# Kernel tuning notes

Hardware: AMD Instinct MI355X
Metric: run time of the kernel (lower is better)

The kernel has to match this reference:

```python
import jax, jax.numpy as jnp
import numpy as np
import math

POOL = 7
NUM_CLASSES = 91
NMS_THRESH = 0.5
SCORE_THRESH = 0.05
TOPK = 100
DW_MAX = math.log(1000.0 / 16)


def _roi_pool(feat, rois, scale):
    # feat [C,H,W]; rois [N,4] xyxy in image coords. Matches torchvision.ops.roi_pool quantization.
    C, H, W = feat.shape
    N = rois.shape[0]
    r = jnp.round(rois * scale)
    x1, y1, x2, y2 = r[:, 0], r[:, 1], r[:, 2], r[:, 3]
    roi_w = jnp.maximum(x2 - x1 + 1.0, 1.0)
    roi_h = jnp.maximum(y2 - y1 + 1.0, 1.0)
    pb = jnp.arange(POOL, dtype=feat.dtype)
    hstart = jnp.clip(jnp.floor(pb[None, :] * roi_h[:, None] / POOL) + y1[:, None], 0, H)
    hend = jnp.clip(jnp.ceil((pb[None, :] + 1) * roi_h[:, None] / POOL) + y1[:, None], 0, H)
    wstart = jnp.clip(jnp.floor(pb[None, :] * roi_w[:, None] / POOL) + x1[:, None], 0, W)
    wend = jnp.clip(jnp.ceil((pb[None, :] + 1) * roi_w[:, None] / POOL) + x1[:, None], 0, W)
    hs = jnp.arange(H, dtype=feat.dtype)
    ws = jnp.arange(W, dtype=feat.dtype)
    mask_h = (hs >= hstart[..., None]) & (hs < hend[..., None])  # [N,P,H]
    mask_w = (ws >= wstart[..., None]) & (ws < wend[..., None])  # [N,P,W]
    NEG = jnp.asarray(-1e30, feat.dtype)

    def pool_one(mh, mw):
        # separable masked max: first over W, then over H
        t = jnp.where(mw[None, None, :, :], feat[:, :, None, :], NEG).max(-1)  # [C,H,P]
        o = jnp.where(mh[None, :, :, None], t[:, None, :, :], NEG).max(2)      # [C,P,P]
        empty = (~mh.any(-1))[:, None] | (~mw.any(-1))[None, :]                 # empty bins -> 0
        return jnp.where(empty[None], jnp.zeros((), feat.dtype), o)

    CH = 8  # chunk proposals to bound peak memory of the [C,H,P,W] intermediate
    mh = mask_h.reshape(N // CH, CH, POOL, H)
    mw = mask_w.reshape(N // CH, CH, POOL, W)
    pooled = jax.lax.map(lambda ms: jax.vmap(pool_one)(ms[0], ms[1]), (mh, mw))
    return pooled.reshape(N, C, POOL, POOL)


def _pairwise_iou(b1, b2):
    a1 = (b1[:, 2] - b1[:, 0]) * (b1[:, 3] - b1[:, 1])
    a2 = (b2[:, 2] - b2[:, 0]) * (b2[:, 3] - b2[:, 1])
    xl = jnp.maximum(b1[:, None, 0], b2[:, 0])
    yt = jnp.maximum(b1[:, None, 1], b2[:, 1])
    xr = jnp.minimum(b1[:, None, 2], b2[:, 2])
    yb = jnp.minimum(b1[:, None, 3], b2[:, 3])
    inter = jnp.maximum(xr - xl, 0.0) * jnp.maximum(yb - yt, 0.0)
    return inter / (a1[:, None] + a2 - inter + 1e-9)


def setup_inputs() -> dict:
    key = jax.random.key(0)
    ks = jax.random.split(key, 10)
    feat = jax.random.normal(ks[0], (1, 256, 50, 50), jnp.float32)
    N = 2000
    cx = jax.random.uniform(ks[1], (N,)) * 800.0
    cy = jax.random.uniform(ks[2], (N,)) * 800.0
    bw = jax.random.uniform(ks[3], (N,)) * 280.0 + 20.0
    bh = jax.random.uniform(ks[4], (N,)) * 280.0 + 20.0
    x1 = jnp.clip(cx - bw / 2, 0.0, 798.0)
    y1 = jnp.clip(cy - bh / 2, 0.0, 798.0)
    x2 = jnp.clip(cx + bw / 2, x1 + 1.0, 800.0)
    y2 = jnp.clip(cy + bh / 2, y1 + 1.0, 800.0)
    proposals = jnp.stack([x1, y1, x2, y2], axis=1).astype(jnp.float32)
    D = 256 * POOL * POOL
    fc1_w = jax.random.normal(ks[5], (1024, D), jnp.float32) * 0.01
    fc2_w = jax.random.normal(ks[6], (1024, 1024), jnp.float32) * 0.01
    cls_w = jax.random.normal(ks[7], (NUM_CLASSES, 1024), jnp.float32) * 0.01
    reg_w = jax.random.normal(ks[8], (NUM_CLASSES * 4, 1024), jnp.float32) * 0.001
    return dict(feat=feat, proposals=proposals,
                fc1_w=fc1_w, fc1_b=jnp.zeros((1024,), jnp.float32),
                fc2_w=fc2_w, fc2_b=jnp.zeros((1024,), jnp.float32),
                cls_w=cls_w, cls_b=jnp.zeros((NUM_CLASSES,), jnp.float32),
                reg_w=reg_w, reg_b=jnp.zeros((NUM_CLASSES * 4,), jnp.float32),
                img_h=800, img_w=800)


def reference(feat, proposals, fc1_w, fc1_b, fc2_w, fc2_b, cls_w, cls_b, reg_w, reg_b, img_h, img_w):
    fmap = feat[0]
    fh, fw = fmap.shape[-2:]
    scale = min(fh / img_h, fw / img_w)
    N = proposals.shape[0]
    pooled = _roi_pool(fmap, proposals, scale).reshape(N, -1)
    x = jax.nn.relu(pooled @ fc1_w.T + fc1_b)
    x = jax.nn.relu(x @ fc2_w.T + fc2_b)
    cls_scores = x @ cls_w.T + cls_b
    reg = (x @ reg_w.T + reg_b).reshape(N, NUM_CLASSES, 4)
    probs = jax.nn.softmax(cls_scores, axis=-1)
    fg = probs[:, 1:]
    pred_scores = fg.max(-1)
    pred_labels = fg.argmax(-1) + 1
    sel = reg[jnp.arange(N), pred_labels]
    pw = proposals[:, 2] - proposals[:, 0]
    ph = proposals[:, 3] - proposals[:, 1]
    pcx = proposals[:, 0] + 0.5 * pw
    pcy = proposals[:, 1] + 0.5 * ph
    dx, dy = sel[:, 0], sel[:, 1]
    dw = jnp.minimum(sel[:, 2], DW_MAX)
    dh = jnp.minimum(sel[:, 3], DW_MAX)
    cx = dx * pw + pcx
    cy = dy * ph + pcy
    bw = jnp.exp(dw) * pw
    bh = jnp.exp(dh) * ph
    boxes = jnp.stack([
        jnp.clip(cx - 0.5 * bw, 0.0, img_w),
        jnp.clip(cy - 0.5 * bh, 0.0, img_h),
        jnp.clip(cx + 0.5 * bw, 0.0, img_w),
        jnp.clip(cy + 0.5 * bh, 0.0, img_h)], axis=1)
    widths = boxes[:, 2] - boxes[:, 0]
    heights = boxes[:, 3] - boxes[:, 1]
    valid = (pred_scores >= SCORE_THRESH) & (widths >= 1.0) & (heights >= 1.0)
    # batched greedy NMS via per-class coordinate offset (torchvision batched_nms)
    sb = jax.lax.stop_gradient(boxes)
    offs = pred_labels.astype(boxes.dtype) * (sb.max() + 1.0)
    ob = sb + offs[:, None]
    order = jnp.argsort(jnp.where(valid, -pred_scores, jnp.inf))
    ob_s = ob[order]
    v_s = valid[order]
    iou = _pairwise_iou(ob_s, ob_s)
    idxs = jnp.arange(N)

    def body(i, supp):
        keep_i = v_s[i] & (~supp[i])
        return supp | (keep_i & (iou[i] > NMS_THRESH) & (idxs > i))

    supp = jax.lax.fori_loop(0, N, body, jnp.zeros((N,), bool))
    keep = v_s & (~supp)
    masked = jnp.where(keep, pred_scores[order], -jnp.inf)
    topv, topi = jax.lax.top_k(masked, TOPK)
    sel_idx = order[topi]
    ok = topv > -jnp.inf
    out_boxes = jnp.where(ok[:, None], boxes[sel_idx], 0.0)
    out_scores = jnp.where(ok, pred_scores[sel_idx], 0.0)
    out_labels = jnp.where(ok, pred_labels[sel_idx], 0)
    return out_boxes, out_labels, out_scores
```

## Files before the change

kernel.cpp:

```cpp
#include <hip/hip_runtime.h>
#include <cstdint>

#define POOLK 7
#define NCLS 91
#define FH 50
#define FW 50
#define FCH 256
#define DIM (FCH * POOLK * POOLK)
#define HID 1024
#define TOPK_OUT 100
#define DW_MAXF 4.135166556742356f

typedef __attribute__((ext_vector_type(8))) short short8;
typedef __attribute__((ext_vector_type(4))) float f32x4;

__device__ __forceinline__ unsigned short f2bf(float x)
{
    unsigned u = __float_as_uint(x);
    return (unsigned short)((u + 0x7FFFu + ((u >> 16) & 1u)) >> 16);
}

__global__ __launch_bounds__(256) void ftrans_kernel(
    const float* __restrict__ feat, float* __restrict__ featT)
{
    __shared__ float tile[64][65];
    int c0 = blockIdx.x * 64;
    int p0 = blockIdx.y * 64;
    int lane = threadIdx.x & 63, r4 = threadIdx.x >> 6;
    #pragma unroll
    for (int r = r4; r < 64; r += 4) {
        int p = p0 + lane;
        if (p < FH * FW) tile[r][lane] = feat[(size_t)(c0 + r) * (FH * FW) + p];
    }
    __syncthreads();
    #pragma unroll
    for (int r = r4; r < 64; r += 4) {
        int p = p0 + r;
        if (p < FH * FW) featT[(size_t)p * FCH + c0 + lane] = tile[lane][r];
    }
}

__global__ __launch_bounds__(512) void roi_pool_kernel(
    const float* __restrict__ featT, const float* __restrict__ props,
    unsigned short* __restrict__ pooled, int n0, int rows,
    const int* __restrict__ img_h, const int* __restrict__ img_w)
{
    int rl = blockIdx.x;
    if (rl >= rows) return;
    int n = n0 + rl;
    int lane = threadIdx.x & 63;
    int wv = threadIdx.x >> 6;

    float scale = (float)fmin((double)FH / (double)img_h[0],
                              (double)FW / (double)img_w[0]);
    float x1 = rintf(props[n * 4 + 0] * scale);
    float y1 = rintf(props[n * 4 + 1] * scale);
    float x2 = rintf(props[n * 4 + 2] * scale);
    float y2 = rintf(props[n * 4 + 3] * scale);
    float roiw = fmaxf(x2 - x1 + 1.f, 1.f);
    float roih = fmaxf(y2 - y1 + 1.f, 1.f);

    const float4* ft4 = (const float4*)featT;
    unsigned short* orow = pooled + (size_t)rl * DIM;

    for (int cell = wv; cell < 49; cell += 8) {
        int py = cell / 7, px = cell - py * 7;
        int h0 = (int)fminf(fmaxf(floorf((float)py * roih / 7.f) + y1, 0.f), (float)FH);
        int h1 = (int)fminf(fmaxf(ceilf(((float)py + 1.f) * roih / 7.f) + y1, 0.f), (float)FH);
        int w0 = (int)fminf(fmaxf(floorf((float)px * roiw / 7.f) + x1, 0.f), (float)FW);
        int w1 = (int)fminf(fmaxf(ceilf(((float)px + 1.f) * roiw / 7.f) + x1, 0.f), (float)FW);

        float4 ma = make_float4(-INFINITY, -INFINITY, -INFINITY, -INFINITY);
        float4 mb = ma;
        for (int h = h0; h < h1; ++h) {
            const float4* rp = ft4 + (size_t)(h * FW) * 64 + lane;
            int w = w0;
            for (; w + 1 < w1; w += 2) {
                float4 va = rp[(size_t)w * 64];
                float4 vb = rp[(size_t)(w + 1) * 64];
                ma.x = fmaxf(ma.x, va.x); ma.y = fmaxf(ma.y, va.y);
                ma.z = fmaxf(ma.z, va.z); ma.w = fmaxf(ma.w, va.w);
                mb.x = fmaxf(mb.x, vb.x); mb.y = fmaxf(mb.y, vb.y);
                mb.z = fmaxf(mb.z, vb.z); mb.w = fmaxf(mb.w, vb.w);
            }
            if (w < w1) {
                float4 va = rp[(size_t)w * 64];
                ma.x = fmaxf(ma.x, va.x); ma.y = fmaxf(ma.y, va.y);
                ma.z = fmaxf(ma.z, va.z); ma.w = fmaxf(ma.w, va.w);
            }
        }
        float4 m;
        m.x = fmaxf(ma.x, mb.x); m.y = fmaxf(ma.y, mb.y);
        m.z = fmaxf(ma.z, mb.z); m.w = fmaxf(ma.w, mb.w);
        if (h0 >= h1 || w0 >= w1) m = make_float4(0.f, 0.f, 0.f, 0.f);
        ushort4 o;
        o.x = f2bf(m.x); o.y = f2bf(m.y); o.z = f2bf(m.z); o.w = f2bf(m.w);
        *(ushort4*)&orow[cell * FCH + lane * 4] = o;
    }
}

__global__ __launch_bounds__(256) void wconv_kernel(
    const float* __restrict__ w, unsigned short* __restrict__ wh, int n4)
{
    int i = blockIdx.x * 256 + threadIdx.x;
    if (i >= n4) return;
    float4 v = ((const float4*)w)[i];
    ushort4 o;
    o.x = f2bf(v.x); o.y = f2bf(v.y); o.z = f2bf(v.z); o.w = f2bf(v.w);
    ((ushort4*)wh)[i] = o;
}

#define PERM_PAD 257
__global__ __launch_bounds__(256) void wconv_perm_kernel(
    const float* __restrict__ w, unsigned short* __restrict__ wh)
{
    __shared__ unsigned short sh[49 * PERM_PAD];
    int n = blockIdx.x;
    const float* row = w + (size_t)n * DIM;
    #pragma unroll 7
    for (int k = 0; k < 49; ++k) {
        int j = k * 256 + threadIdx.x;
        float v = row[j];
        int c = j / 49, cell = j - c * 49;
        sh[cell * PERM_PAD + c] = f2bf(v);
    }
    __syncthreads();
    unsigned short* orow = wh + (size_t)n * DIM;
    #pragma unroll 7
    for (int k = 0; k < 49; ++k) {
        int o = k * 256 + threadIdx.x;
        int cell = o >> 8, c = o & 255;
        orow[o] = sh[cell * PERM_PAD + c];
    }
}

#define GBM 128
#define GBN 128
#define GBK 64

typedef __attribute__((address_space(1))) void* gas_p;
typedef __attribute__((address_space(3))) void* las_p;
__device__ __forceinline__ void async16(void* l, const void* g)
{
    __builtin_amdgcn_global_load_lds((gas_p)g, (las_p)l, 16, 0, 0);
}

__global__ __launch_bounds__(256, 2) void gemm_bf16_kernel(
    const unsigned short* __restrict__ A, const unsigned short* __restrict__ B,
    float* __restrict__ part, int M, int N, int K, int ksteps, int KS)
{
    __shared__ unsigned short ldsA[2][GBM * GBK];
    __shared__ unsigned short ldsB[2][GBN * GBK];

    int t = threadIdx.x;
    int lane = t & 63, wave = t >> 6;
    int m0 = blockIdx.y * GBM, n0 = blockIdx.x * GBN;

    int steps_per = (ksteps + KS - 1) / KS;
    int ks0 = blockIdx.z * steps_per;
    int ks1 = min(ksteps, ks0 + steps_per);
    int nt = ks1 - ks0;

    int lrow  = lane >> 3;
    int lslot = (lane & 7) ^ lrow;
    const unsigned short* aSrc[4];
    const unsigned short* bSrc[4];
    #pragma unroll
    for (int i = 0; i < 4; ++i) {
        int r = wave * 32 + i * 8 + lrow;
        int gm = min(m0 + r, M - 1);
        int gn = min(n0 + r, N - 1);
        aSrc[i] = A + (size_t)gm * K + lslot * 8;
        bSrc[i] = B + (size_t)gn * K + lslot * 8;
    }

    int wr = wave >> 1, wc = wave & 1;
    int fr = lane & 15, fq = lane >> 4;

    f32x4 acc[4][4] = {};

    auto STAGE = [&](int buf, int kt) {
        int koff = kt * GBK;
        #pragma unroll
        for (int i = 0; i < 4; ++i) {
            async16(&ldsA[buf][(wave * 32 + i * 8) * GBK], aSrc[i] + koff);
            async16(&ldsB[buf][(wave * 32 + i * 8) * GBK], bSrc[i] + koff);
        }
    };

    auto COMPUTE = [&](int buf) {
        #pragma unroll
        for (int h = 0; h < 2; ++h) {
            short8 af[4], bfr[4];
            #pragma unroll
            for (int mi = 0; mi < 4; ++mi) {
                int r = wr * 64 + mi * 16 + fr;
                int idx = r * GBK + (((h * 4 + fq) ^ (r & 7)) << 3);
                af[mi] = *(const short8*)&ldsA[buf][idx];
            }
            #pragma unroll
            for (int ni = 0; ni < 4; ++ni) {
                int r = wc * 64 + ni * 16 + fr;
                int idx = r * GBK + (((h * 4 + fq) ^ (r & 7)) << 3);
                bfr[ni] = *(const short8*)&ldsB[buf][idx];
            }
            #pragma unroll
            for (int mi = 0; mi < 4; ++mi)
                #pragma unroll
                for (int ni = 0; ni < 4; ++ni)
                    acc[mi][ni] = __builtin_amdgcn_mfma_f32_16x16x32_bf16(
                        af[mi], bfr[ni], acc[mi][ni], 0, 0, 0);
        }
    };

    if (nt > 0) STAGE(0, ks0);
    __syncthreads();
    int cur = 0;
    for (int ts = 0; ts < nt; ++ts) {
        if (ts + 1 < nt) STAGE(cur ^ 1, ks0 + ts + 1);
        COMPUTE(cur);
        __syncthreads();
        cur ^= 1;
    }

    float* pbase = part + (size_t)blockIdx.z * M * N;
    #pragma unroll
    for (int mi = 0; mi < 4; ++mi) {
        #pragma unroll
        for (int ni = 0; ni < 4; ++ni) {
            int col = n0 + wc * 64 + ni * 16 + fr;
            if (col >= N) continue;
            #pragma unroll
            for (int j = 0; j < 4; ++j) {
                int row = m0 + wr * 64 + mi * 16 + fq * 4 + j;
                if (row < M) pbase[(size_t)row * N + col] = acc[mi][ni][j];
            }
        }
    }
}

__global__ __launch_bounds__(256) void reduce_kernel(
    const float* __restrict__ part, const float* __restrict__ bias,
    float* __restrict__ outf, unsigned short* __restrict__ outh,
    int M, int N, int KS, int relu)
{
    int idx = blockIdx.x * 256 + threadIdx.x;
    int tot = M * N;
    if (idx >= tot) return;
    int n = idx % N;
    float s = 0.f;
    for (int k = 0; k < KS; ++k) s += part[(size_t)k * tot + idx];
    s += bias[n];
    if (relu) s = fmaxf(s, 0.f);
    if (outf) outf[idx] = s;
    if (outh) outh[idx] = f2bf(s);
}

__global__ __launch_bounds__(256) void decode_kernel(
    const float* __restrict__ cls, const float* __restrict__ x2buf,
    const float* __restrict__ reg_w, const float* __restrict__ reg_b,
    const float* __restrict__ props,
    float* __restrict__ scores, int* __restrict__ labels,
    float* __restrict__ boxes, int* __restrict__ valid,
    int n0, int rows, const int* __restrict__ img_h, const int* __restrict__ img_w)
{
    int rl = blockIdx.x;
    if (rl >= rows) return;
    int r = n0 + rl;
    int t = threadIdx.x;
    int lane = t & 63, wv = t >> 6;

    __shared__ float s_score;
    __shared__ int s_label;
    __shared__ float s_dsum[4];

    if (wv == 0) {
        float v0 = (lane < NCLS) ? cls[(size_t)r * NCLS + lane] : -INFINITY;
        float v1 = (lane + 64 < NCLS) ? cls[(size_t)r * NCLS + lane + 64] : -INFINITY;

        float mall = fmaxf(v0, v1);
        for (int s = 32; s; s >>= 1) mall = fmaxf(mall, __shfl_xor(mall, s));

        float bv = -INFINITY; int bi = 1 << 30;
        if (lane >= 1 && lane < NCLS) { bv = v0; bi = lane; }
        if (lane + 64 < NCLS && v1 > bv) { bv = v1; bi = lane + 64; }
        for (int s = 32; s; s >>= 1) {
            float ov = __shfl_xor(bv, s); int oi = __shfl_xor(bi, s);
            if (ov > bv || (ov == bv && oi < bi)) { bv = ov; bi = oi; }
        }

        float den = ((lane < NCLS) ? expf(v0 - mall) : 0.f) +
                    ((lane + 64 < NCLS) ? expf(v1 - mall) : 0.f);
        for (int s = 32; s; s >>= 1) den += __shfl_xor(den, s);

        if (lane == 0) {
            s_score = expf(bv - mall) / den;
            s_label = bi;
        }
    }
    __syncthreads();
    int label = s_label;

    {
        const float4* xr4 = (const float4*)(x2buf + (size_t)rl * HID);
        const float4* wr4 = (const float4*)(reg_w + (size_t)(label * 4 + wv) * HID);
        float4 a0 = xr4[lane],        b0 = wr4[lane];
        float4 a1 = xr4[lane + 64],   b1 = wr4[lane + 64];
        float4 a2 = xr4[lane + 128],  b2 = wr4[lane + 128];
        float4 a3 = xr4[lane + 192],  b3 = wr4[lane + 192];
        float sA = 0.f, sB = 0.f;
        sA = fmaf(a0.x, b0.x, sA); sA = fmaf(a0.y, b0.y, sA);
        sA = fmaf(a0.z, b0.z, sA); sA = fmaf(a0.w, b0.w, sA);
        sB = fmaf(a1.x, b1.x, sB); sB = fmaf(a1.y, b1.y, sB);
        sB = fmaf(a1.z, b1.z, sB); sB = fmaf(a1.w, b1.w, sB);
        sA = fmaf(a2.x, b2.x, sA); sA = fmaf(a2.y, b2.y, sA);
        sA = fmaf(a2.z, b2.z, sA); sA = fmaf(a2.w, b2.w, sA);
        sB = fmaf(a3.x, b3.x, sB); sB = fmaf(a3.y, b3.y, sB);
        sB = fmaf(a3.z, b3.z, sB); sB = fmaf(a3.w, b3.w, sB);
        float s = sA + sB;
        for (int sh = 32; sh; sh >>= 1) s += __shfl_xor(s, sh);
        if (lane == 0) s_dsum[wv] = s + reg_b[label * 4 + wv];
    }
    __syncthreads();

    if (t == 0) {
        float score = s_score;
        float p0 = props[r * 4 + 0], p1 = props[r * 4 + 1];
        float p2 = props[r * 4 + 2], p3 = props[r * 4 + 3];
        float pw = p2 - p0, ph = p3 - p1;
        float pcx = p0 + 0.5f * pw, pcy = p1 + 0.5f * ph;
        float dx = s_dsum[0], dy = s_dsum[1];
        float dw = fminf(s_dsum[2], DW_MAXF), dh = fminf(s_dsum[3], DW_MAXF);
        float cx = dx * pw + pcx, cy = dy * ph + pcy;
        float bw = expf(dw) * pw, bh = expf(dh) * ph;
        float iw = (float)img_w[0], ih = (float)img_h[0];
        float b0 = fminf(fmaxf(cx - 0.5f * bw, 0.f), iw);
        float b1 = fminf(fmaxf(cy - 0.5f * bh, 0.f), ih);
        float b2 = fminf(fmaxf(cx + 0.5f * bw, 0.f), iw);
        float b3 = fminf(fmaxf(cy + 0.5f * bh, 0.f), ih);
        boxes[r * 4 + 0] = b0; boxes[r * 4 + 1] = b1;
        boxes[r * 4 + 2] = b2; boxes[r * 4 + 3] = b3;
        scores[r] = score; labels[r] = label;
        valid[r] = (score >= 0.05f) && (b2 - b0 >= 1.f) && (b3 - b1 >= 1.f);
    }
}

__global__ __launch_bounds__(1024) void gmax_kernel(
    const float* __restrict__ boxes, unsigned int* __restrict__ gmax, int total)
{
    int t = threadIdx.x;
    float m = -INFINITY;
    for (int i = t; i < total; i += 1024) m = fmaxf(m, boxes[i]);
    for (int s = 32; s; s >>= 1) m = fmaxf(m, __shfl_xor(m, s));
    __shared__ float wm[16];
    if ((t & 63) == 0) wm[t >> 6] = m;
    __syncthreads();
    if (t < 16) {
        float v = wm[t];
        for (int s = 8; s; s >>= 1) v = fmaxf(v, __shfl_xor(v, s));
        if (t == 0) gmax[0] = __float_as_uint(v);
    }
}

__global__ __launch_bounds__(256) void rank_kernel(
    const float* __restrict__ scores, const int* __restrict__ valid,
    int* __restrict__ order, int N)
{
    int i = blockIdx.x * 256 + threadIdx.x;
    __shared__ float sk[256];
    float ki = INFINITY;
    if (i < N && valid[i]) ki = -scores[i];
    int rank = 0;
    for (int j0 = 0; j0 < N; j0 += 256) {
        int j = j0 + threadIdx.x;
        float kj = INFINITY;
        if (j < N && valid[j]) kj = -scores[j];
        __syncthreads();
        sk[threadIdx.x] = kj;
        __syncthreads();
        int lim = min(256, N - j0);
        for (int jj = 0; jj < lim; ++jj) {
            float k2 = sk[jj];
            int jidx = j0 + jj;
            rank += (k2 < ki) || (k2 == ki && jidx < i);
        }
    }
    if (i < N) order[rank] = i;
}

__global__ __launch_bounds__(256) void sortprep_kernel(
    const int* __restrict__ order, const float* __restrict__ boxes,
    const float* __restrict__ scores, const int* __restrict__ labels,
    const int* __restrict__ valid, const unsigned int* __restrict__ gmax,
    float* __restrict__ sob, float* __restrict__ sarea,
    float* __restrict__ sraw, float* __restrict__ ssc, int* __restrict__ slb,
    int* __restrict__ vcount, int N)
{
    int i = blockIdx.x * 256 + threadIdx.x;
    bool v = false;
    if (i < N) {
        int oi = order[i];
        float off = (float)labels[oi] * (__uint_as_float(gmax[0]) + 1.0f);
        float b0 = boxes[oi * 4 + 0] + off, b1 = boxes[oi * 4 + 1] + off;
        float b2 = boxes[oi * 4 + 2] + off, b3 = boxes[oi * 4 + 3] + off;
        sob[i * 4 + 0] = b0; sob[i * 4 + 1] = b1; sob[i * 4 + 2] = b2; sob[i * 4 + 3] = b3;
        sarea[i] = (b2 - b0) * (b3 - b1);
        sraw[i * 4 + 0] = boxes[oi * 4 + 0]; sraw[i * 4 + 1] = boxes[oi * 4 + 1];
        sraw[i * 4 + 2] = boxes[oi * 4 + 2]; sraw[i * 4 + 3] = boxes[oi * 4 + 3];
        ssc[i] = scores[oi]; slb[i] = labels[oi];
        v = valid[oi] != 0;
    }
    unsigned long long b = __ballot(v);
    if ((threadIdx.x & 63) == 0 && b)
        atomicAdd(vcount, __popcll(b));
}

__global__ __launch_bounds__(256) void mask_kernel(
    const float* __restrict__ sob, const float* __restrict__ sarea,
    const int* __restrict__ vcount,
    unsigned long long* __restrict__ mask, int N, int NW)
{
    int V = vcount[0];
    int t = threadIdx.x;
    int w = t & 31, il = t >> 5;
    int i = blockIdx.x * 8 + il;
    if (i >= V || w >= NW) return;
    int jbase = w * 64;
    if (jbase >= V) return;
    float4 bi = *(const float4*)(sob + (size_t)i * 4);
    float ai = sarea[i];
    unsigned long long bits = 0;
    for (int b = 0; b < 64; ++b) {
        int j = jbase + b;
        if (j > i && j < V) {
            float4 bj = *(const float4*)(sob + (size_t)j * 4);
            float xl = fmaxf(bi.x, bj.x), yt = fmaxf(bi.y, bj.y);
            float xr = fminf(bi.z, bj.z), yb = fminf(bi.w, bj.w);
            float inter = fmaxf(xr - xl, 0.f) * fmaxf(yb - yt, 0.f);
            float iou = inter / (ai + sarea[j] - inter + 1e-9f);
            if (iou > 0.5f) bits |= 1ull << b;
        }
    }
    mask[(size_t)i * NW + w] = bits;
}

__global__ __launch_bounds__(64) void nms_kernel(
    const unsigned long long* __restrict__ mask,
    const int* __restrict__ vcount,
    const float* __restrict__ sraw, const float* __restrict__ ssc,
    const int* __restrict__ slb, float* __restrict__ out, int N, int NW)
{
    int V = vcount[0];
    int NWv = (V + 63) >> 6;
    int lane = threadIdx.x;
    unsigned long long supp = 0;
    int cnt = 0;
    for (int i = 0; i < V && cnt < TOPK_OUT; ++i) {
        int w = i >> 6, b = i & 63;
        unsigned long long sw = __shfl(supp, w);
        if (!((sw >> b) & 1ull)) {
            unsigned long long mi =
                (lane < NWv) ? mask[(size_t)i * NW + lane] : 0ull;
            supp |= mi;
            if (lane < 4) out[cnt * 4 + lane] = sraw[i * 4 + lane];
            if (lane == 4) out[4 * TOPK_OUT + cnt] = (float)slb[i];
            if (lane == 5) out[5 * TOPK_OUT + cnt] = ssc[i];
            cnt++;
        }
    }
    for (int s = cnt; s < TOPK_OUT; ++s) {
        if (lane < 4) out[s * 4 + lane] = 0.f;
        if (lane == 4) out[4 * TOPK_OUT + s] = 0.f;
        if (lane == 5) out[5 * TOPK_OUT + s] = 0.f;
    }
}

extern "C" void kernel_launch(void* const* d_in, const int* in_sizes, int n_in,
                              void* d_out, int out_size, void* d_ws, size_t ws_size,
                              hipStream_t stream)
{
    const float* feat  = (const float*)d_in[0];
    const float* props = (const float*)d_in[1];
    const float* fc1_w = (const float*)d_in[2];
    const float* fc1_b = (const float*)d_in[3];
    const float* fc2_w = (const float*)d_in[4];
    const float* fc2_b = (const float*)d_in[5];
    const float* cls_w = (const float*)d_in[6];
    const float* cls_b = (const float*)d_in[7];
    const float* reg_w = (const float*)d_in[8];
    const float* reg_b = (const float*)d_in[9];
    const int* img_h = (const int*)d_in[10];
    const int* img_w = (const int*)d_in[11];
    float* out = (float*)d_out;

    int N = in_sizes[1] / 4;
    int NW = (N + 63) >> 6;
    int n_fc1w = in_sizes[2];
    int n_fc2w = in_sizes[4];
    int n_clsw = in_sizes[6];

    auto al = [](size_t x) { return (x + 255) & ~(size_t)255; };

    size_t miscBytes =
        al((size_t)FH * FW * FCH * 4) +
        al((size_t)N * NCLS * 4) +
        al((size_t)N * 4) * 6 +
        al((size_t)N * 16) * 3 +
        al((size_t)N * 4) +
        al(4) + al(4) +
        al((size_t)N * NW * 8);
    size_t wBytes = al((size_t)n_fc1w * 2) + al((size_t)n_fc2w * 2) +
                    al((size_t)n_clsw * 2);

    size_t partCap = 32u << 20;
    int chunk = N;
    auto need = [&](int ch, size_t pc) {
        return al(pc) + wBytes + miscBytes +
               al((size_t)ch * DIM * 2) +
               al((size_t)ch * HID * 2) +
               al((size_t)ch * HID * 4) +
               al((size_t)ch * HID * 2);
    };
    while (need(chunk, partCap) > ws_size && chunk > 125) chunk = (chunk + 1) / 2;
    while (need(chunk, partCap) > ws_size && partCap > ((size_t)chunk * HID * 4 + (4u<<20)))
        partCap >>= 1;

    char* p = (char*)d_ws;
    auto grab = [&](size_t bytes) { char* q = p; p += al(bytes); return q; };
    float* part = (float*)grab(partCap);
    unsigned short* fc1wh = (unsigned short*)grab((size_t)n_fc1w * 2);
    unsigned short* fc2wh = (unsigned short*)grab((size_t)n_fc2w * 2);
    unsigned short* clswh = (unsigned short*)grab((size_t)n_clsw * 2);
    unsigned short* pooledh = (unsigned short*)grab((size_t)chunk * DIM * 2);
    unsigned short* x1h = (unsigned short*)grab((size_t)chunk * HID * 2);
    float* x2f = (float*)grab((size_t)chunk * HID * 4);
    unsigned short* x2h = (unsigned short*)grab((size_t)chunk * HID * 2);
    float* featT  = (float*)grab((size_t)FH * FW * FCH * 4);
    float* cls    = (float*)grab((size_t)N * NCLS * 4);
    float* scores = (float*)grab((size_t)N * 4);
    int*   labels = (int*)grab((size_t)N * 4);
    int*   valid  = (int*)grab((size_t)N * 4);
    float* boxes  = (float*)grab((size_t)N * 16);
    int*   order  = (int*)grab((size_t)N * 4);
    float* sob    = (float*)grab((size_t)N * 16);
    float* sarea  = (float*)grab((size_t)N * 4);
    float* sraw   = (float*)grab((size_t)N * 16);
    float* ssc    = (float*)grab((size_t)N * 4);
    int*   slb    = (int*)grab((size_t)N * 4);
    int*   vcount = (int*)grab(4);
    unsigned int* gmax = (unsigned int*)grab(4);
    unsigned long long* maskp = (unsigned long long*)grab((size_t)N * NW * 8);

    hipMemsetAsync(vcount, 0, 4, stream);

    {
        dim3 g(FCH / 64, (FH * FW + 63) / 64);
        ftrans_kernel<<<g, 256, 0, stream>>>(feat, featT);
    }
    wconv_perm_kernel<<<HID, 256, 0, stream>>>(fc1_w, fc1wh);
    wconv_kernel<<<(n_fc2w / 4 + 255) / 256, 256, 0, stream>>>(fc2_w, fc2wh, n_fc2w / 4);
    wconv_kernel<<<(n_clsw / 4 + 255) / 256, 256, 0, stream>>>(cls_w, clswh, n_clsw / 4);

    auto gemmb = [&](const unsigned short* Ah, const unsigned short* Bh,
                     const float* bias, float* outf, unsigned short* outh,
                     int M_, int N_, int K_, int relu) {
        int gm = (M_ + GBM - 1) / GBM;
        int gn = (N_ + GBN - 1) / GBN;
        int ksteps = K_ / GBK;
        int KS = 512 / (gm * gn);
        if (KS < 1) KS = 1;
        if (KS > 16) KS = 16;
        long ksMem = (long)(partCap / ((size_t)M_ * N_ * 4));
        if (KS > ksMem) KS = (int)ksMem;
        if (KS > ksteps) KS = ksteps;
        if (KS < 1) KS = 1;
        dim3 g(gn, gm, KS);
        gemm_bf16_kernel<<<g, 256, 0, stream>>>(Ah, Bh, part, M_, N_, K_, ksteps, KS);
        int tot = M_ * N_;
        reduce_kernel<<<(tot + 255) / 256, 256, 0, stream>>>(part, bias, outf, outh,
                                                             M_, N_, KS, relu);
    };

    for (int n0 = 0; n0 < N; n0 += chunk) {
        int rows = min(chunk, N - n0);
        roi_pool_kernel<<<rows, 512, 0, stream>>>(
            featT, props, pooledh, n0, rows, img_h, img_w);
        gemmb(pooledh, fc1wh, fc1_b, nullptr, x1h, rows, HID, DIM, 1);
        gemmb(x1h, fc2wh, fc2_b, x2f, x2h, rows, HID, HID, 1);
        gemmb(x2h, clswh, cls_b, cls + (size_t)n0 * NCLS, nullptr, rows, NCLS, HID, 0);
        decode_kernel<<<rows, 256, 0, stream>>>(
            cls, x2f, reg_w, reg_b, props, scores, labels, boxes, valid,
            n0, rows, img_h, img_w);
    }

    gmax_kernel<<<1, 1024, 0, stream>>>(boxes, gmax, N * 4);
    rank_kernel<<<(N + 255) / 256, 256, 0, stream>>>(scores, valid, order, N);
    sortprep_kernel<<<(N + 255) / 256, 256, 0, stream>>>(
        order, boxes, scores, labels, valid, gmax, sob, sarea, sraw, ssc, slb,
        vcount, N);
    mask_kernel<<<(N + 7) / 8, 256, 0, stream>>>(sob, sarea, vcount, maskp, N, NW);
    nms_kernel<<<1, 64, 0, stream>>>(maskp, vcount, sraw, ssc, slb, out, N, NW);
}
```

Before: 373.4 us.

## Add 256x256-tile GEMM for fc1 and store split-K partials in bf16

Adds a 512-thread GEMM kernel with 256x256 output tiles and 8 waves. It is used for large-K, wide-N layers (fc1), where it halves the split-K fan-out. Split-K partial sums in both GEMMs are now written as bf16 instead of fp32, which halves partial-buffer write and reduce-read traffic. The larger tile uses 128KB of LDS, so it likely gets only one block per CU. Rounding the partials to bf16 before summing adds accumulation error.

```diff
diff --git a/kernel.cpp b/kernel.cpp
--- a/kernel.cpp
+++ b/kernel.cpp
@@ -18,6 +18,10 @@
 {
     unsigned u = __float_as_uint(x);
     return (unsigned short)((u + 0x7FFFu + ((u >> 16) & 1u)) >> 16);
+}
+__device__ __forceinline__ float bf2f(unsigned short h)
+{
+    return __uint_as_float((unsigned)h << 16);
 }
 
 __global__ __launch_bounds__(256) void ftrans_kernel(
@@ -134,10 +138,6 @@
     }
 }
 
-#define GBM 128
-#define GBN 128
-#define GBK 64
-
 typedef __attribute__((address_space(1))) void* gas_p;
 typedef __attribute__((address_space(3))) void* las_p;
 __device__ __forceinline__ void async16(void* l, const void* g)
@@ -145,16 +145,17 @@
     __builtin_amdgcn_global_load_lds((gas_p)g, (las_p)l, 16, 0, 0);
 }
 
+#define GBK 64
 __global__ __launch_bounds__(256, 2) void gemm_bf16_kernel(
     const unsigned short* __restrict__ A, const unsigned short* __restrict__ B,
-    float* __restrict__ part, int M, int N, int K, int ksteps, int KS)
-{
-    __shared__ unsigned short ldsA[2][GBM * GBK];
-    __shared__ unsigned short ldsB[2][GBN * GBK];
+    unsigned short* __restrict__ part, int M, int N, int K, int ksteps, int KS)
+{
+    __shared__ unsigned short ldsA[2][128 * GBK];
+    __shared__ unsigned short ldsB[2][128 * GBK];
 
     int t = threadIdx.x;
     int lane = t & 63, wave = t >> 6;
-    int m0 = blockIdx.y * GBM, n0 = blockIdx.x * GBN;
+    int m0 = blockIdx.y * 128, n0 = blockIdx.x * 128;
 
     int steps_per = (ksteps + KS - 1) / KS;
     int ks0 = blockIdx.z * steps_per;
@@ -223,7 +224,7 @@
         cur ^= 1;
     }
 
-    float* pbase = part + (size_t)blockIdx.z * M * N;
+    unsigned short* pbase = part + (size_t)blockIdx.z * M * N;
     #pragma unroll
     for (int mi = 0; mi < 4; ++mi) {
         #pragma unroll
@@ -233,14 +234,108 @@
             #pragma unroll
             for (int j = 0; j < 4; ++j) {
                 int row = m0 + wr * 64 + mi * 16 + fq * 4 + j;
-                if (row < M) pbase[(size_t)row * N + col] = acc[mi][ni][j];
+                if (row < M) pbase[(size_t)row * N + col] = f2bf(acc[mi][ni][j]);
             }
         }
     }
 }
 
+__global__ __launch_bounds__(512, 2) void gemm256_bf16_kernel(
+    const unsigned short* __restrict__ A, const unsigned short* __restrict__ B,
+    unsigned short* __restrict__ part, int M, int N, int K, int ksteps, int KS)
+{
+    __shared__ unsigned short ldsA[2][256 * GBK];
+    __shared__ unsigned short ldsB[2][256 * GBK];
+
+    int t = threadIdx.x;
+    int lane = t & 63, wave = t >> 6;
+    int m0 = blockIdx.y * 256, n0 = blockIdx.x * 256;
+
+    int steps_per = (ksteps + KS - 1) / KS;
+    int ks0 = blockIdx.z * steps_per;
+    int ks1 = min(ksteps, ks0 + steps_per);
+    int nt = ks1 - ks0;
+
+    int lrow  = lane >> 3;
+    int lslot = (lane & 7) ^ lrow;
+    const unsigned short* aSrc[4];
+    const unsigned short* bSrc[4];
+    #pragma unroll
+    for (int i = 0; i < 4; ++i) {
+        int r = wave * 32 + i * 8 + lrow;
+        int gm = min(m0 + r, M - 1);
+        int gn = min(n0 + r, N - 1);
+        aSrc[i] = A + (size_t)gm * K + lslot * 8;
+        bSrc[i] = B + (size_t)gn * K + lslot * 8;
+    }
+
+    int wr = wave >> 2, wc = wave & 3;
+    int fr = lane & 15, fq = lane >> 4;
+
+    f32x4 acc[8][4] = {};
+
+    auto STAGE = [&](int buf, int kt) {
+        int koff = kt * GBK;
+        #pragma unroll
+        for (int i = 0; i < 4; ++i) {
+            async16(&ldsA[buf][(wave * 32 + i * 8) * GBK], aSrc[i] + koff);
+            async16(&ldsB[buf][(wave * 32 + i * 8) * GBK], bSrc[i] + koff);
+        }
+    };
+
+    auto COMPUTE = [&](int buf) {
+        #pragma unroll
+        for (int h = 0; h < 2; ++h) {
+            short8 af[8], bfr[4];
+            #pragma unroll
+            for (int mi = 0; mi < 8; ++mi) {
+                int r = wr * 128 + mi * 16 + fr;
+                int idx = r * GBK + (((h * 4 + fq) ^ (r & 7)) << 3);
+                af[mi] = *(const short8*)&ldsA[buf][idx];
+            }
+            #pragma unroll
+            for (int ni = 0; ni < 4; ++ni) {
+                int r = wc * 64 + ni * 16 + fr;
+                int idx = r * GBK + (((h * 4 + fq) ^ (r & 7)) << 3);
+                bfr[ni] = *(const short8*)&ldsB[buf][idx];
+            }
+            #pragma unroll
+            for (int mi = 0; mi < 8; ++mi)
+                #pragma unroll
+                for (int ni = 0; ni < 4; ++ni)
+                    acc[mi][ni] = __builtin_amdgcn_mfma_f32_16x16x32_bf16(
+                        af[mi], bfr[ni], acc[mi][ni], 0, 0, 0);
+        }
+    };
+
+    if (nt > 0) STAGE(0, ks0);
+    __syncthreads();
+    int cur = 0;
+    for (int ts = 0; ts < nt; ++ts) {
+        if (ts + 1 < nt) STAGE(cur ^ 1, ks0 + ts + 1);
+        COMPUTE(cur);
+        __syncthreads();
+        cur ^= 1;
+    }
+
+    unsigned short* pbase = part + (size_t)blockIdx.z * M * N;
+    #pragma unroll
+    for (int mi = 0; mi < 8; ++mi) {
+        #pragma unroll
+        for (int ni = 0; ni < 4; ++ni) {
+            int col = n0 + wc * 64 + ni * 16 + fr;
+            if (col >= N) continue;
+            #pragma unroll
+            for (int j = 0; j < 4; ++j) {
+                int row = m0 + wr * 128 + mi * 16 + fq * 4 + j;
+                if (row < M) pbase[(size_t)row * N + col] = f2bf(acc[mi][ni][j]);
+            }
+        }
+    }
+}
+
 __global__ __launch_bounds__(256) void reduce_kernel(
-    const float* __restrict__ part, const float* __restrict__ bias,
+    const unsigned short* __restrict__ part, const float* __restrict__ bias,
     float* __restrict__ outf, unsigned short* __restrict__ outh,
     int M, int N, int KS, int relu)
 {
@@ -249,7 +344,7 @@
     if (idx >= tot) return;
     int n = idx % N;
     float s = 0.f;
-    for (int k = 0; k < KS; ++k) s += part[(size_t)k * tot + idx];
+    for (int k = 0; k < KS; ++k) s += bf2f(part[(size_t)k * tot + idx]);
     s += bias[n];
     if (relu) s = fmaxf(s, 0.f);
     if (outf) outf[idx] = s;
@@ -522,12 +617,12 @@
                al((size_t)ch * HID * 2);
     };
     while (need(chunk, partCap) > ws_size && chunk > 125) chunk = (chunk + 1) / 2;
-    while (need(chunk, partCap) > ws_size && partCap > ((size_t)chunk * HID * 4 + (4u<<20)))
+    while (need(chunk, partCap) > ws_size && partCap > ((size_t)chunk * HID * 2 + (4u<<20)))
         partCap >>= 1;
 
     char* p = (char*)d_ws;
     auto grab = [&](size_t bytes) { char* q = p; p += al(bytes); return q; };
-    float* part = (float*)grab(partCap);
+    unsigned short* part = (unsigned short*)grab(partCap);
     unsigned short* fc1wh = (unsigned short*)grab((size_t)n_fc1w * 2);
     unsigned short* fc2wh = (unsigned short*)grab((size_t)n_fc2w * 2);
     unsigned short* clswh = (unsigned short*)grab((size_t)n_clsw * 2);
@@ -564,18 +659,25 @@
     auto gemmb = [&](const unsigned short* Ah, const unsigned short* Bh,
                      const float* bias, float* outf, unsigned short* outh,
                      int M_, int N_, int K_, int relu) {
-        int gm = (M_ + GBM - 1) / GBM;
-        int gn = (N_ + GBN - 1) / GBN;
+        bool big = (K_ >= 4096) && (N_ >= 256);
+        int BT = big ? 256 : 128;
+        int gm = (M_ + BT - 1) / BT;
+        int gn = (N_ + BT - 1) / BT;
         int ksteps = K_ / GBK;
-        int KS = 512 / (gm * gn);
+        int KS = (big ? 256 : 512) / (gm * gn);
         if (KS < 1) KS = 1;
         if (KS > 16) KS = 16;
-        long ksMem = (long)(partCap / ((size_t)M_ * N_ * 4));
+        long ksMem = (long)(partCap / ((size_t)M_ * N_ * 2));
         if (KS > ksMem) KS = (int)ksMem;
         if (KS > ksteps) KS = ksteps;
         if (KS < 1) KS = 1;
         dim3 g(gn, gm, KS);
-        gemm_bf16_kernel<<<g, 256, 0, stream>>>(Ah, Bh, part, M_, N_, K_, ksteps, KS);
+        if (big)
+            gemm256_bf16_kernel<<<g, 512, 0, stream>>>(Ah, Bh, part, M_, N_, K_,
+                                                       ksteps, KS);
+        else
+            gemm_bf16_kernel<<<g, 256, 0, stream>>>(Ah, Bh, part, M_, N_, K_,
+                                                    ksteps, KS);
         int tot = M_ * N_;
         reduce_kernel<<<(tot + 255) / 256, 256, 0, stream>>>(part, bias, outf, outh,
                                                              M_, N_, KS, relu);
```

Result: no change. 367.6 us (-1.6%).
